# Kernel optimization log

Hardware: AMD Instinct MI355X
Metric: run time of the kernel (lower is better)

Reference implementation:

```python
import jax, jax.numpy as jnp
import numpy as np

N = 100000        # num nodes
D = 128           # emb_dim
EH = 400000       # half-edge count (E // 2)
H = 64            # mlp_edge_model_dim
TEMP = 1.0        # b_temp
BIAS = 1e-4       # concrete-relaxation bias (0.0 + 0.0001)


def _xavier(key, shape):
    fan_in, fan_out = shape
    lim = float(np.sqrt(6.0 / (fan_in + fan_out)))
    return jax.random.uniform(key, shape, jnp.float32, -lim, lim)


def setup_inputs() -> dict:
    key = jax.random.key(0)
    ks = jax.random.split(key, 7)
    node_emb = jax.random.normal(ks[0], (N, D), jnp.float32)
    src = jax.random.randint(ks[1], (EH,), 0, N, jnp.int64)
    dst = jax.random.randint(ks[2], (EH,), 0, N, jnp.int64)
    vals = jax.random.uniform(ks[3], (EH,), jnp.float32)
    eps_u = jax.random.uniform(ks[4], (EH, 1), jnp.float32)  # torch.rand noise
    W1 = _xavier(ks[5], (2 * D, H))
    b1 = jnp.zeros((H,), jnp.float32)
    W2 = _xavier(ks[6], (H, 1))
    b2 = jnp.zeros((1,), jnp.float32)
    return {"node_emb": node_emb, "src": src, "dst": dst, "vals": vals,
            "eps_u": eps_u, "W1": W1, "b1": b1, "W2": W2, "b2": b2}


def reference(node_emb, src, dst, vals, eps_u, W1, b1, W2, b2):
    # gather + concat: [EH, 2D]
    edge_emb = jnp.concatenate([node_emb[src], node_emb[dst]], axis=1)
    # 2-layer MLP -> edge logits [EH, 1]
    h = jax.nn.relu(edge_emb @ W1 + b1)
    edge_logits = h @ W2 + b2
    # concrete / gumbel-sigmoid gate
    eps = (BIAS - (1.0 - BIAS)) * eps_u + (1.0 - BIAS)  # in [BIAS, 1-BIAS]
    gate_inputs = (jnp.log(eps) - jnp.log1p(-eps) + edge_logits) / TEMP
    aug_edge_weight = jax.nn.sigmoid(gate_inputs)[:, 0]  # [EH]
    mean_edge_weight = jnp.sum(aug_edge_weight) / EH
    new_vals = vals * aug_edge_weight
    # n_adj + n_adj.T: uncoalesced COO concat -> duplicated values; the
    # symmetric index list is concat([src, dst]), concat([dst, src]).
    sym_vals = jnp.concatenate([new_vals, new_vals])  # [2*EH]
    return (sym_vals, mean_edge_weight)
```

## Files before the change

### kernel.cpp

```cpp
#include <hip/hip_runtime.h>
#include <hip/hip_bf16.h>

#define NN 100000
#define DD 128
#define EHn 400000
#define BIASc 1e-4f
#define NBLK_EDGE 1563

using bf16x8 = __attribute__((ext_vector_type(8))) __bf16;
using f32x4  = __attribute__((ext_vector_type(4))) float;

#define PQ_OFF    0
#define PQ_BYTES  ((size_t)NN * DD * 2)
#define PART_OFF  PQ_BYTES

__global__ __launch_bounds__(256)
void node_proj_kernel(const float* __restrict__ emb, const float* __restrict__ W1,
                      const float* __restrict__ b1, __bf16* __restrict__ PQ) {
    __shared__ __bf16 sfrag[16384];
    #pragma unroll
    for (int i = 0; i < 8; ++i) {
        int e = threadIdx.x + i * 256;
        int l = e & 63;
        int f = (e >> 6) & 7;
        int t = e >> 9;
        int c = f * 16 + (l & 15);
        const float* wcol = (c < 64) ? (W1 + c) : (W1 + 128 * 64 + (c - 64));
        int kbase = t * 32 + ((l >> 4) << 3);
        bf16x8 v;
        #pragma unroll
        for (int j = 0; j < 8; ++j)
            v[j] = (__bf16)wcol[(kbase + j) * 64];
        *(bf16x8*)(&sfrag[(size_t)e * 8]) = v;
    }
    __syncthreads();

    const int lane = threadIdx.x & 63;
    const int wave = threadIdx.x >> 6;
    const int rowBase = blockIdx.x * 128 + wave * 32;
    const int r16 = lane & 15;
    const int kg  = lane >> 4;

    f32x4 acc[2][8];
    #pragma unroll
    for (int m = 0; m < 2; ++m)
        #pragma unroll
        for (int f = 0; f < 8; ++f)
            acc[m][f] = (f32x4){0.f, 0.f, 0.f, 0.f};

    const bf16x8* sfragV = (const bf16x8*)sfrag;

    #pragma unroll
    for (int t = 0; t < 4; ++t) {
        bf16x8 af[2];
        #pragma unroll
        for (int m = 0; m < 2; ++m) {
            int row = rowBase + m * 16 + r16;
            row = row < NN ? row : NN - 1;
            const float* ap = emb + (size_t)row * DD + t * 32 + kg * 8;
            float4 lo = *(const float4*)ap;
            float4 hi = *(const float4*)(ap + 4);
            bf16x8 v;
            v[0] = (__bf16)lo.x; v[1] = (__bf16)lo.y; v[2] = (__bf16)lo.z; v[3] = (__bf16)lo.w;
            v[4] = (__bf16)hi.x; v[5] = (__bf16)hi.y; v[6] = (__bf16)hi.z; v[7] = (__bf16)hi.w;
            af[m] = v;
        }
        #pragma unroll
        for (int f = 0; f < 8; ++f) {
            bf16x8 bf = sfragV[(t * 8 + f) * 64 + lane];
            #pragma unroll
            for (int m = 0; m < 2; ++m)
                acc[m][f] = __builtin_amdgcn_mfma_f32_16x16x32_bf16(af[m], bf, acc[m][f], 0, 0, 0);
        }
    }

    #pragma unroll
    for (int m = 0; m < 2; ++m) {
        #pragma unroll
        for (int f = 0; f < 8; ++f) {
            #pragma unroll
            for (int r = 0; r < 4; ++r) {
                int row = rowBase + m * 16 + kg * 4 + r;
                int col = f * 16 + r16;
                float v = acc[m][f][r];
                if (col < 64) v += b1[col];
                if (row < NN) PQ[(size_t)row * DD + col] = (__bf16)v;
            }
        }
    }
}

__global__ __launch_bounds__(256)
void edge_kernel(const __bf16* __restrict__ PQ, const int* __restrict__ src,
                 const int* __restrict__ dst, const float* __restrict__ vals,
                 const float* __restrict__ eps_u, const float* __restrict__ W2,
                 const float* __restrict__ b2, float* __restrict__ out,
                 float* __restrict__ partials) {
    const int e = blockIdx.x * 256 + threadIdx.x;
    float wgate = 0.f;

    if (e < EHn) {
        const int s = src[e];
        const int d = dst[e];
        const uint4* prow = (const uint4*)(PQ + (size_t)s * DD);
        const uint4* qrow = (const uint4*)(PQ + (size_t)d * DD + 64);

        float acc0 = 0.f, acc1 = 0.f;
        #pragma unroll
        for (int c = 0; c < 8; ++c) {
            uint4 p = prow[c];
            uint4 q = qrow[c];
            const unsigned pw[4] = {p.x, p.y, p.z, p.w};
            const unsigned qw[4] = {q.x, q.y, q.z, q.w};
            #pragma unroll
            for (int k = 0; k < 4; ++k) {
                int i = c * 8 + k * 2;
                float pl = __uint_as_float(pw[k] << 16);
                float ph = __uint_as_float(pw[k] & 0xffff0000u);
                float ql = __uint_as_float(qw[k] << 16);
                float qh = __uint_as_float(qw[k] & 0xffff0000u);
                acc0 = fmaf(fmaxf(pl + ql, 0.f), W2[i], acc0);
                acc1 = fmaf(fmaxf(ph + qh, 0.f), W2[i + 1], acc1);
            }
        }
        float logit = acc0 + acc1 + b2[0];

        float u = eps_u[e];
        float epsv = fmaf(2.f * BIASc - 1.f, u, 1.f - BIASc);
        float ome  = fmaf(1.f - 2.f * BIASc, u, BIASc);
        float g = __logf(epsv) - __logf(ome) + logit;
        wgate = 1.f / (1.f + __expf(-g));
        float nv = vals[e] * wgate;
        out[e] = nv;
        out[EHn + e] = nv;
    }

    __shared__ float sred[256];
    sred[threadIdx.x] = wgate;
    __syncthreads();
    #pragma unroll
    for (int st = 128; st >= 64; st >>= 1) {
        if ((int)threadIdx.x < st) sred[threadIdx.x] += sred[threadIdx.x + st];
        __syncthreads();
    }
    if (threadIdx.x < 64) {
        float a = sred[threadIdx.x];
        #pragma unroll
        for (int off = 32; off > 0; off >>= 1)
            a += __shfl_xor(a, off, 64);
        if (threadIdx.x == 0) partials[blockIdx.x] = a;
    }
}

__global__ void mean_kernel(const float* __restrict__ partials, float* __restrict__ out) {
    __shared__ float s[256];
    float a = 0.f;
    for (int i = threadIdx.x; i < NBLK_EDGE; i += 256) a += partials[i];
    s[threadIdx.x] = a;
    __syncthreads();
    for (int st = 128; st > 0; st >>= 1) {
        if ((int)threadIdx.x < st) s[threadIdx.x] += s[threadIdx.x + st];
        __syncthreads();
    }
    if (threadIdx.x == 0) out[2 * EHn] = s[0] / (float)EHn;
}

extern "C" void kernel_launch(void* const* d_in, const int* in_sizes, int n_in,
                              void* d_out, int out_size, void* d_ws, size_t ws_size,
                              hipStream_t stream) {
    const float* emb  = (const float*)d_in[0];
    const int*   src  = (const int*)d_in[1];
    const int*   dst  = (const int*)d_in[2];
    const float* vals = (const float*)d_in[3];
    const float* eps  = (const float*)d_in[4];
    const float* W1   = (const float*)d_in[5];
    const float* b1   = (const float*)d_in[6];
    const float* W2   = (const float*)d_in[7];
    const float* b2   = (const float*)d_in[8];
    float* out = (float*)d_out;

    char* ws = (char*)d_ws;
    __bf16* PQ       = (__bf16*)(ws + PQ_OFF);
    float*  partials = (float*)(ws + PART_OFF);

    hipLaunchKernelGGL(node_proj_kernel, dim3((NN + 127) / 128), dim3(256), 0, stream,
                       emb, W1, b1, PQ);
    hipLaunchKernelGGL(edge_kernel, dim3(NBLK_EDGE), dim3(256), 0, stream,
                       PQ, src, dst, vals, eps, W2, b2, out, partials);
    hipLaunchKernelGGL(mean_kernel, dim3(1), dim3(256), 0, stream, partials, out);
}
```

Before: 52.28 us.

## Split each edge's gathered row across 8 lanes for coalesced loads

The edge kernel now assigns 8 lanes per edge, with each lane loading one 16-byte chunk of the P and Q rows and reducing the partial dot product via shuffles. Previously one thread walked the full 128-byte rows serially, so each load instruction was scattered across a wave. Adjacent lanes now read contiguous memory, which should use cache lines better and put more loads in flight. The cost is shuffle reductions and only one lane in eight doing the gate math and stores, which gives less coalesced output writes.

```diff
diff --git a/kernel.cpp b/kernel.cpp
--- a/kernel.cpp
+++ b/kernel.cpp
@@ -96,47 +96,61 @@
                  const float* __restrict__ eps_u, const float* __restrict__ W2,
                  const float* __restrict__ b2, float* __restrict__ out,
                  float* __restrict__ partials) {
-    const int e = blockIdx.x * 256 + threadIdx.x;
-    float wgate = 0.f;
-
-    if (e < EHn) {
-        const int s = src[e];
-        const int d = dst[e];
-        const uint4* prow = (const uint4*)(PQ + (size_t)s * DD);
-        const uint4* qrow = (const uint4*)(PQ + (size_t)d * DD + 64);
-
-        float acc0 = 0.f, acc1 = 0.f;
-        #pragma unroll
-        for (int c = 0; c < 8; ++c) {
-            uint4 p = prow[c];
-            uint4 q = qrow[c];
-            const unsigned pw[4] = {p.x, p.y, p.z, p.w};
-            const unsigned qw[4] = {q.x, q.y, q.z, q.w};
-            #pragma unroll
-            for (int k = 0; k < 4; ++k) {
-                int i = c * 8 + k * 2;
-                float pl = __uint_as_float(pw[k] << 16);
-                float ph = __uint_as_float(pw[k] & 0xffff0000u);
-                float ql = __uint_as_float(qw[k] << 16);
-                float qh = __uint_as_float(qw[k] & 0xffff0000u);
-                acc0 = fmaf(fmaxf(pl + ql, 0.f), W2[i], acc0);
-                acc1 = fmaf(fmaxf(ph + qh, 0.f), W2[i + 1], acc1);
-            }
-        }
-        float logit = acc0 + acc1 + b2[0];
-
-        float u = eps_u[e];
-        float epsv = fmaf(2.f * BIASc - 1.f, u, 1.f - BIASc);
-        float ome  = fmaf(1.f - 2.f * BIASc, u, BIASc);
-        float g = __logf(epsv) - __logf(ome) + logit;
-        wgate = 1.f / (1.f + __expf(-g));
-        float nv = vals[e] * wgate;
-        out[e] = nv;
-        out[EHn + e] = nv;
+    const int lane = threadIdx.x & 63;
+    const int wv   = threadIdx.x >> 6;
+    const int k    = lane & 7;
+    const int g    = lane >> 3;
+
+    float4 wa = *(const float4*)(W2 + k * 8);
+    float4 wb = *(const float4*)(W2 + k * 8 + 4);
+    const float w2v[8] = {wa.x, wa.y, wa.z, wa.w, wb.x, wb.y, wb.z, wb.w};
+    const float b2s = b2[0];
+
+    const int waveBase = blockIdx.x * 256 + wv * 64;
+    float wsum = 0.f;
+
+    #pragma unroll
+    for (int pass = 0; pass < 8; ++pass) {
+        const int e = waveBase + pass * 8 + g;
+        const bool valid = e < EHn;
+        const int s = valid ? src[e] : 0;
+        const int d = valid ? dst[e] : 0;
+
+        uint4 p = *(const uint4*)(PQ + (size_t)s * DD + k * 8);
+        uint4 q = *(const uint4*)(PQ + (size_t)d * DD + 64 + k * 8);
+
+        const unsigned pw[4] = {p.x, p.y, p.z, p.w};
+        const unsigned qw[4] = {q.x, q.y, q.z, q.w};
+        float acc = 0.f;
+        #pragma unroll
+        for (int w = 0; w < 4; ++w) {
+            float pl = __uint_as_float(pw[w] << 16);
+            float ph = __uint_as_float(pw[w] & 0xffff0000u);
+            float ql = __uint_as_float(qw[w] << 16);
+            float qh = __uint_as_float(qw[w] & 0xffff0000u);
+            acc = fmaf(fmaxf(pl + ql, 0.f), w2v[w * 2], acc);
+            acc = fmaf(fmaxf(ph + qh, 0.f), w2v[w * 2 + 1], acc);
+        }
+        acc += __shfl_xor(acc, 1, 64);
+        acc += __shfl_xor(acc, 2, 64);
+        acc += __shfl_xor(acc, 4, 64);
+
+        if (k == 0 && valid) {
+            float logit = acc + b2s;
+            float u = eps_u[e];
+            float epsv = fmaf(2.f * BIASc - 1.f, u, 1.f - BIASc);
+            float ome  = fmaf(1.f - 2.f * BIASc, u, BIASc);
+            float gg = __logf(epsv) - __logf(ome) + logit;
+            float wgate = 1.f / (1.f + __expf(-gg));
+            float nv = vals[e] * wgate;
+            out[e] = nv;
+            out[EHn + e] = nv;
+            wsum += wgate;
+        }
     }
 
     __shared__ float sred[256];
-    sred[threadIdx.x] = wgate;
+    sred[threadIdx.x] = wsum;
     __syncthreads();
     #pragma unroll
     for (int st = 128; st >= 64; st >>= 1) {
```

Result: faster. 46.99 us (-10.1%).
